# Kernel optimization log

Measured on AMD Instinct MI355X. Metric: run time of the kernel, lower is better.

Reference implementation:

```python
import jax, jax.numpy as jnp
import numpy as np

# dims
B, T1, T2, SEG = 4, 16, 16, 4          # batch, src len, tgt len, max segment length
V, E, H, ENC = 8000, 256, 256, 512     # vocab, embed, lstm hidden, encoder units
EOS = 2                                 # end-of-segment symbol ($)
NEG = -1e30                             # finite -inf (grad-safe)


def setup_inputs():
    key = jax.random.key(0)
    ks = jax.random.split(key, 16)
    s = 0.05
    n = lambda k, shp: (jax.random.normal(k, shp) * s).astype(jnp.float32)
    return {
        "prev_output_tokens": jax.random.randint(ks[0], (B, T2), 0, V),
        "encoder_outs": jax.random.normal(ks[1], (T1, B, ENC), dtype=jnp.float32),
        "embed": n(ks[2], (V, E)),
        "start_embed": n(ks[3], (E,)),
        "proj_h_w": n(ks[4], (H, ENC)), "proj_h_b": jnp.zeros((H,), jnp.float32),
        "proj_c_w": n(ks[5], (H, ENC)), "proj_c_b": jnp.zeros((H,), jnp.float32),
        "w_ih0": n(ks[6], (4 * H, H + E)), "w_hh0": n(ks[7], (4 * H, H)), "b0": jnp.zeros((4 * H,), jnp.float32),
        "w_ih1": n(ks[8], (4 * H, H)), "w_hh1": n(ks[9], (4 * H, H)), "b1": jnp.zeros((4 * H,), jnp.float32),
        "fc_w": n(ks[10], (V, H)), "fc_b": jnp.zeros((V,), jnp.float32),
    }


def _lstm_cell(x, h, c, w_ih, w_hh, b):
    # PyTorch LSTMCell gate order: i, f, g, o
    g = x @ w_ih.T + h @ w_hh.T + b
    i, f, gg, o = jnp.split(g, 4, axis=-1)
    c_new = jax.nn.sigmoid(f) * c + jax.nn.sigmoid(i) * jnp.tanh(gg)
    h_new = jax.nn.sigmoid(o) * jnp.tanh(c_new)
    return h_new, c_new


def reference(prev_output_tokens, encoder_outs, embed, start_embed,
              proj_h_w, proj_h_b, proj_c_w, proj_c_b,
              w_ih0, w_hh0, b0, w_ih1, w_hh1, b1, fc_w, fc_b):
    y = prev_output_tokens                                     # [B, T2]
    # segment windows: tok[b, t2, k] = y[b, t2+k] (clipped; masked later via logpy mask)
    pos = jnp.arange(T2 + 1)[:, None] + jnp.arange(SEG)[None, :]   # [T2+1, SEG]
    tok = y[:, jnp.minimum(pos, T2 - 1)]                            # [B, T2+1, SEG]
    emb_tok = embed[tok]                                            # [B, T2+1, SEG, E]
    x0 = jnp.broadcast_to(start_embed, (B, T2 + 1, 1, E))
    xs = jnp.moveaxis(jnp.concatenate([x0, emb_tok], axis=2), 2, 0)  # [SEG+1, B, T2+1, E]
    tgt = jnp.concatenate([tok, jnp.zeros((B, T2 + 1, 1), tok.dtype)], axis=2)
    tgt = jnp.moveaxis(tgt, 2, 0)                                    # [SEG+1, B, T2+1]

    # per-encoder-position initial states / context (encoder proj, as in __init__)
    eo = jnp.swapaxes(encoder_outs, 0, 1)                            # [B, T1, ENC]
    h0 = eo @ proj_h_w.T + proj_h_b                                  # [B, T1, H]
    c0 = eo @ proj_c_w.T + proj_c_b
    ctx = jnp.broadcast_to(h0[:, :, None, :], (B, T1, T2 + 1, H))

    def step(carry, inp):
        h1, c1, h2, c2 = carry
        x, t = inp                                                   # x [B,T2+1,E], t [B,T2+1]
        xb = jnp.broadcast_to(x[:, None, :, :], (B, T1, T2 + 1, E))
        h1, c1 = _lstm_cell(jnp.concatenate([ctx, xb], axis=-1), h1, c1, w_ih0, w_hh0, b0)
        h2, c2 = _lstm_cell(h1, h2, c2, w_ih1, w_hh1, b1)
        logp = jax.nn.log_softmax(h2 @ fc_w.T + fc_b, axis=-1)       # [B,T1,T2+1,V]
        idx = jnp.broadcast_to(t[:, None, :, None], (B, T1, T2 + 1, 1))
        sel = jnp.take_along_axis(logp, idx, axis=-1)[..., 0]
        return (h1, c1, h2, c2), (sel, logp[..., EOS])

    carry0 = (ctx,
              jnp.broadcast_to(c0[:, :, None, :], (B, T1, T2 + 1, H)),
              jnp.zeros((B, T1, T2 + 1, H), jnp.float32),
              jnp.zeros((B, T1, T2 + 1, H), jnp.float32))
    _, (sel, eosp) = jax.lax.scan(step, carry0, (xs, tgt))           # each [SEG+1,B,T1,T2+1]

    # logpy[b,t1,t2,j] = sum_{k<j} logp_k(y[t2+k]) + logp_j(EOS)
    cum = jnp.concatenate([jnp.zeros((1, B, T1, T2 + 1), sel.dtype),
                           jnp.cumsum(sel[:SEG], axis=0)], axis=0)
    logpy = jnp.moveaxis(cum + eosp, 0, -1)                          # [B,T1,T2+1,SEG+1]
    jmask = (jnp.arange(T2 + 1)[:, None] + jnp.arange(SEG + 1)[None, :]) <= T2
    logpy = jnp.where(jmask[None, None], logpy, NEG)

    # semi-Markov forward DP: alpha[t1+1, t2] = LSE_j alpha[t1, t2-j] + logpy[t1, t2-j, j]
    alpha0 = jnp.full((B, T2 + 1), NEG, sel.dtype).at[:, 0].set(0.0)

    def dp(alpha, row):                                              # row [B, T2+1, SEG+1]
        v = alpha[:, :, None] + row
        shifted = jnp.stack(
            [jnp.pad(v[:, :T2 + 1 - j, j], ((0, 0), (j, 0)), constant_values=NEG)
             for j in range(SEG + 1)], axis=0)
        return jax.nn.logsumexp(shifted, axis=0), None

    alpha, _ = jax.lax.scan(dp, alpha0, jnp.moveaxis(logpy, 1, 0))
    return alpha[:, T2]                                              # log-likelihood per batch elem
```

## Files before the change

kernel.cpp:

```cpp
#include <hip/hip_runtime.h>
#include <math.h>

#define B 4
#define T1 16
#define T2 16
#define SEG 4
#define V 8000
#define E 256
#define H 256
#define ENC 512
#define EOS 2
#define NEGV -1e30f
#define G4 1024
#define NCELL 1088
#define T21 17
#define NL 272
#define MROWS 5440
#define NFCT 10625

typedef __attribute__((ext_vector_type(4))) float f32x4;
typedef __attribute__((ext_vector_type(8))) short bf16x8;

__device__ __forceinline__ float sigm(float x) { return 1.f / (1.f + __expf(-x)); }
__device__ __forceinline__ float ftanh(float x) { float e = __expf(2.f * x); return 1.f - 2.f / (e + 1.f); }
__device__ __forceinline__ float b2f(short x) {
    unsigned u = ((unsigned)(unsigned short)x) << 16;
    return __builtin_bit_cast(float, u);
}
__device__ __forceinline__ short f2b(float f) {
    unsigned u = __builtin_bit_cast(unsigned, f);
    unsigned r = (u + 0x7fffu + ((u >> 16) & 1u)) >> 16;
    return (short)r;
}

__device__ __forceinline__ void stage64(const char* g0, size_t gstrideB, int kOffB, char* lds) {
    int tid = threadIdx.x;
#pragma unroll
    for (int it = 0; it < 8; ++it) {
        int chunk = it * 256 + tid;
        int row = chunk >> 5;
        int c16 = chunk & 31;
        const char* src = g0 + (size_t)row * gstrideB + kOffB + ((c16 ^ (row & 7)) << 4);
        __builtin_amdgcn_global_load_lds((const __attribute__((address_space(1))) void*)src,
                                         (__attribute__((address_space(3))) void*)(lds + chunk * 16),
                                         16, 0, 0);
    }
}

__device__ __forceinline__ bf16x8 lds_frag(const char* lds, int row, int col16) {
    return *(const bf16x8*)(lds + row * 512 + ((col16 ^ (row & 7)) << 4));
}

__device__ __forceinline__ void mma_tile(const char* smA, const char* smB,
                                         int wave, int ln, int kg, f32x4 acc[4]) {
#pragma unroll
    for (int ks = 0; ks < 8; ++ks) {
        bf16x8 a = lds_frag(smA, wave * 16 + ln, ks * 4 + kg);
#pragma unroll
        for (int nf = 0; nf < 4; ++nf) {
            bf16x8 b = lds_frag(smB, nf * 16 + ln, ks * 4 + kg);
            acc[nf] = __builtin_amdgcn_mfma_f32_16x16x32_bf16(a, b, acc[nf], 0, 0, 0);
        }
    }
}

__global__ void k_setup(const float* __restrict__ fcw, const float* __restrict__ whh0,
                        const float* __restrict__ wih1, const float* __restrict__ whh1,
                        const float* __restrict__ phw, const float* __restrict__ pcw,
                        const float* __restrict__ wih0, const float* __restrict__ b1,
                        short* __restrict__ fcwbf, short* __restrict__ whh0i, short* __restrict__ w1i,
                        float* __restrict__ projhT, float* __restrict__ projcT,
                        float* __restrict__ ctxT, float* __restrict__ xT, float* __restrict__ b1i) {
    int bid = blockIdx.x, tid = threadIdx.x;
    if (bid < 8000) { int i = bid * 256 + tid; fcwbf[i] = f2b(fcw[i]); return; }
    bid -= 8000;
    if (bid < 1024) {
        int i = bid * 256 + tid; int gp = i >> 8, k = i & 255; int j = gp >> 2, gate = gp & 3;
        whh0i[i] = f2b(whh0[(size_t)(gate * 256 + j) * 256 + k]); return;
    }
    bid -= 1024;
    if (bid < 2048) {
        int i = bid * 256 + tid; int gp = i >> 9, k = i & 511; int j = gp >> 2, gate = gp & 3;
        float v = (k < 256) ? wih1[(size_t)(gate * 256 + j) * 256 + k]
                            : whh1[(size_t)(gate * 256 + j) * 256 + (k - 256)];
        w1i[i] = f2b(v); return;
    }
    bid -= 2048;
    if (bid < 512) { int i = bid * 256 + tid; int k = i >> 8, r = i & 255; projhT[i] = phw[(size_t)r * ENC + k]; return; }
    bid -= 512;
    if (bid < 512) { int i = bid * 256 + tid; int k = i >> 8, r = i & 255; projcT[i] = pcw[(size_t)r * ENC + k]; return; }
    bid -= 512;
    if (bid < 2048) {
        int i = bid * 256 + tid; int g = i >> 9, k = i & 511; float v = wih0[i];
        if (k < 256) ctxT[(size_t)k * G4 + g] = v; else xT[(size_t)(k - 256) * G4 + g] = v;
        return;
    }
    bid -= 2048;
    if (bid < 4) { int i = bid * 256 + tid; int j = i >> 2, gate = i & 3; b1i[i] = b1[gate * 256 + j]; return; }
}

__global__ void k_init_state(const float* __restrict__ enc, const float* __restrict__ phT,
                             const float* __restrict__ phb, const float* __restrict__ pcT,
                             const float* __restrict__ pcb, float* __restrict__ h0, float* __restrict__ c0) {
    __shared__ float eo[ENC];
    int bi = blockIdx.x;
    int b = bi / T1, i = bi % T1;
    int j = threadIdx.x;
    for (int e = j; e < ENC; e += 256) eo[e] = enc[(size_t)(i * B + b) * ENC + e];
    __syncthreads();
    float ha = phb[j], ca = pcb[j];
    for (int e = 0; e < ENC; ++e) {
        float x = eo[e];
        ha += x * phT[(size_t)e * H + j];
        ca += x * pcT[(size_t)e * H + j];
    }
    h0[(size_t)bi * H + j] = ha;
    c0[(size_t)bi * H + j] = ca;
}

__global__ void k_init2(const int* __restrict__ y, const float* __restrict__ embed, const float* __restrict__ se,
                        const float* __restrict__ h0, const float* __restrict__ c0,
                        const float* __restrict__ ctxT, const float* __restrict__ xT,
                        const float* __restrict__ b0,
                        float* __restrict__ c1, float* __restrict__ c2,
                        short* __restrict__ hcA, short* __restrict__ hcB,
                        float* __restrict__ pre_ctxi, float* __restrict__ pre_xi) {
    __shared__ float sb[256];
    int bid = blockIdx.x, j = threadIdx.x;
    if (bid < NCELL) {
        int cell = bid, bi = cell / T21;
        c1[(size_t)cell * H + j] = c0[(size_t)bi * H + j];
        c2[(size_t)cell * H + j] = 0.f;
        hcA[(size_t)cell * 512 + j] = f2b(h0[(size_t)bi * H + j]);
        hcB[(size_t)cell * 512 + 256 + j] = 0;
        return;
    }
    bid -= NCELL;
    if (bid < 64) {
        int bi = bid;
        sb[j] = h0[(size_t)bi * H + j];
        __syncthreads();
        float a0 = b0[j], a1 = b0[256 + j], a2 = b0[512 + j], a3 = b0[768 + j];
        for (int k = 0; k < H; ++k) {
            float x = sb[k];
            const float* w = ctxT + (size_t)k * G4;
            a0 += x * w[j]; a1 += x * w[256 + j]; a2 += x * w[512 + j]; a3 += x * w[768 + j];
        }
        *(float4*)&pre_ctxi[(size_t)bi * G4 + 4 * j] = make_float4(a0, a1, a2, a3);
        return;
    }
    bid -= 64;
    int row = bid;
    int s = row / (B * T21), rem = row % (B * T21);
    int b = rem / T21, t = rem % T21;
    const float* src;
    if (s == 0) src = se;
    else { int tt = t + s - 1; if (tt > 15) tt = 15; src = embed + (size_t)y[b * T2 + tt] * E; }
    sb[j] = src[j];
    __syncthreads();
    float a0 = 0, a1 = 0, a2 = 0, a3 = 0;
    for (int k = 0; k < E; ++k) {
        float x = sb[k];
        const float* w = xT + (size_t)k * G4;
        a0 += x * w[j]; a1 += x * w[256 + j]; a2 += x * w[512 + j]; a3 += x * w[768 + j];
    }
    *(float4*)&pre_xi[(size_t)row * G4 + 4 * j] = make_float4(a0, a1, a2, a3);
}

__device__ __forceinline__ void lstm0_body(int step, int l, char* smA, char* smB,
        const short* __restrict__ IN, const short* __restrict__ whh0i,
        const float* __restrict__ pre_ctxi, const float* __restrict__ pre_xi,
        float* __restrict__ c1, short* __restrict__ OUT) {
    int tid = threadIdx.x;
    int wave = tid >> 6, lane = tid & 63, ln = lane & 15, kg = lane >> 4;
    int mb = l >> 4, nb = l & 15;
    int m0 = mb * 64, n0 = nb * 64;
    stage64((const char*)(IN + (size_t)m0 * 512), 1024, 0, smA);
    stage64((const char*)(whh0i + (size_t)n0 * 256), 512, 0, smB);
    __syncthreads();
    f32x4 acc[4] = {};
    mma_tile(smA, smB, wave, ln, kg, acc);
    __syncthreads();
    float* sg = (float*)smA;
#pragma unroll
    for (int nf = 0; nf < 4; ++nf)
#pragma unroll
        for (int r = 0; r < 4; ++r)
            sg[(wave * 16 + kg * 4 + r) * 68 + nf * 16 + ln] = acc[nf][r];
    __syncthreads();
    int jlo = nb * 16;
#pragma unroll
    for (int q2 = 0; q2 < 4; ++q2) {
        int item = q2 * 256 + tid;
        int c = item >> 4, jj = item & 15;
        int cell = m0 + c;
        int j = jlo + jj;
        float4 g = *(float4*)&sg[c * 68 + 4 * jj];
        int bi = cell / T21;
        int bb = bi >> 4;
        int t = cell % T21;
        int prow = (step * B + bb) * T21 + t;
        float4 pc = *(const float4*)&pre_ctxi[(size_t)bi * G4 + 4 * j];
        float4 px = *(const float4*)&pre_xi[(size_t)prow * G4 + 4 * j];
        float ig = g.x + pc.x + px.x, fg = g.y + pc.y + px.y;
        float gg = g.z + pc.z + px.z, og = g.w + pc.w + px.w;
        float cold = c1[(size_t)cell * H + j];
        float cn = sigm(fg) * cold + sigm(ig) * ftanh(gg);
        float hn = sigm(og) * ftanh(cn);
        c1[(size_t)cell * H + j] = cn;
        OUT[(size_t)cell * 512 + j] = f2b(hn);
    }
}

__device__ __forceinline__ void lstm1_body(int l, char* smA, char* smB,
        const short* __restrict__ IN, const short* __restrict__ w1i,
        const float* __restrict__ b1i, float* __restrict__ c2,
        short* __restrict__ slab, short* __restrict__ OUT) {
    int tid = threadIdx.x;
    int wave = tid >> 6, lane = tid & 63, ln = lane & 15, kg = lane >> 4;
    int mb = l >> 4, nb = l & 15;
    int m0 = mb * 64, n0 = nb * 64;
    f32x4 acc[4] = {};
#pragma unroll
    for (int kh = 0; kh < 2; ++kh) {
        if (kh) __syncthreads();
        stage64((const char*)(IN + (size_t)m0 * 512), 1024, kh * 512, smA);
        stage64((const char*)(w1i + (size_t)n0 * 512), 1024, kh * 512, smB);
        __syncthreads();
        mma_tile(smA, smB, wave, ln, kg, acc);
    }
    __syncthreads();
    float* sg = (float*)smA;
#pragma unroll
    for (int nf = 0; nf < 4; ++nf)
#pragma unroll
        for (int r = 0; r < 4; ++r)
            sg[(wave * 16 + kg * 4 + r) * 68 + nf * 16 + ln] = acc[nf][r];
    __syncthreads();
    int jlo = nb * 16;
#pragma unroll
    for (int q2 = 0; q2 < 4; ++q2) {
        int item = q2 * 256 + tid;
        int c = item >> 4, jj = item & 15;
        int cell = m0 + c;
        int j = jlo + jj;
        float4 g = *(float4*)&sg[c * 68 + 4 * jj];
        float4 bv = *(const float4*)&b1i[4 * j];
        float ig = g.x + bv.x, fg = g.y + bv.y, gg = g.z + bv.z, og = g.w + bv.w;
        float cold = c2[(size_t)cell * H + j];
        float cn = sigm(fg) * cold + sigm(ig) * ftanh(gg);
        float hn = sigm(og) * ftanh(cn);
        c2[(size_t)cell * H + j] = cn;
        short hb = f2b(hn);
        slab[(size_t)cell * 256 + j] = hb;
        OUT[(size_t)cell * 512 + 256 + j] = hb;
    }
}

__global__ __launch_bounds__(256, 2) void k_lstm(int s, int n_l1,
        const short* __restrict__ IN, short* __restrict__ OUT, short* __restrict__ slab,
        const short* __restrict__ whh0i, const short* __restrict__ w1i,
        const float* __restrict__ pre_ctxi, const float* __restrict__ pre_xi,
        const float* __restrict__ b1i, float* __restrict__ c1, float* __restrict__ c2) {
    __shared__ char smem[65536];
    char* smA = smem;
    char* smB = smem + 32768;
    int bx = blockIdx.x;
    if (bx < n_l1) lstm1_body(bx, smA, smB, IN, w1i, b1i, c2, slab, OUT);
    else lstm0_body(s + 1, bx - n_l1, smA, smB, IN, whh0i, pre_ctxi, pre_xi, c1, OUT);
}

__global__ __launch_bounds__(256, 2) void k_fc(const short* __restrict__ h2base, const short* __restrict__ Wv,
        const float* __restrict__ fcb, float* __restrict__ psum) {
    __shared__ char smem[65536];
    char* smA = smem;
    char* smB = smem + 32768;
    int bx = blockIdx.x;
    int xcd = bx & 7, idx = bx >> 3;
    int q = NFCT >> 3, r = NFCT & 7;
    int l = xcd * q + (xcd < r ? xcd : r) + idx;
    int nb = l / 85, rem = l % 85;
    int s = rem / 17, mb = rem % 17;
    int m0 = s * NCELL + mb * 64;
    int n0 = nb * 64;
    int tid = threadIdx.x;
    int wave = tid >> 6, lane = tid & 63, ln = lane & 15, kg = lane >> 4;
    stage64((const char*)(h2base + (size_t)m0 * 256), 512, 0, smA);
    stage64((const char*)(Wv + (size_t)n0 * 256), 512, 0, smB);
    __syncthreads();
    f32x4 acc[4] = {};
    mma_tile(smA, smB, wave, ln, kg, acc);
    float rs[4] = {0.f, 0.f, 0.f, 0.f};
#pragma unroll
    for (int nf = 0; nf < 4; ++nf) {
        float fbn = fcb[n0 + nf * 16 + ln];
#pragma unroll
        for (int r2 = 0; r2 < 4; ++r2)
            rs[r2] += __expf(acc[nf][r2] + fbn);
    }
#pragma unroll
    for (int mask = 1; mask < 16; mask <<= 1)
#pragma unroll
        for (int r2 = 0; r2 < 4; ++r2)
            rs[r2] += __shfl_xor(rs[r2], mask);
    if (ln == 0) {
#pragma unroll
        for (int r2 = 0; r2 < 4; ++r2)
            psum[(size_t)nb * MROWS + m0 + wave * 16 + kg * 4 + r2] = rs[r2];
    }
}

__global__ void k_combine(const short* __restrict__ h2all, const short* __restrict__ Wv,
        const float* __restrict__ fcb, const int* __restrict__ y,
        const float* __restrict__ psum, float* __restrict__ sel, float* __restrict__ eosp) {
    int cb = blockIdx.x;
    int s = cb / 17, blk = cb % 17;
    int tid = threadIdx.x;
    int cl = tid >> 2, q = tid & 3;
    int cell = blk * 64 + cl;
    int b = cell / (T1 * T21);
    int t = cell % T21;
    int tv = 0;
    if (s < SEG) { int tt = t + s; if (tt > 15) tt = 15; tv = y[b * T2 + tt]; }
    const short* hp = h2all + (size_t)(s + 1) * NCELL * 256 + (size_t)cell * 256 + q * 64;
    const short* w1 = Wv + (size_t)tv * 256 + q * 64;
    const short* w2 = Wv + (size_t)EOS * 256 + q * 64;
    float d1 = 0.f, d2 = 0.f;
#pragma unroll
    for (int u = 0; u < 8; ++u) {
        bf16x8 av  = *(const bf16x8*)(hp + u * 8);
        bf16x8 wv1 = *(const bf16x8*)(w1 + u * 8);
        bf16x8 wv2 = *(const bf16x8*)(w2 + u * 8);
#pragma unroll
        for (int e = 0; e < 8; ++e) {
            float a = b2f(av[e]);
            d1 += a * b2f(wv1[e]);
            d2 += a * b2f(wv2[e]);
        }
    }
    d1 += __shfl_xor(d1, 1); d1 += __shfl_xor(d1, 2);
    d2 += __shfl_xor(d2, 1); d2 += __shfl_xor(d2, 2);
    int col = s * NCELL + cell;
    float ss = 0.f;
    for (int v2 = q * 32; v2 < q * 32 + 32 && v2 < 125; ++v2)
        ss += psum[(size_t)v2 * MROWS + col];
    ss += __shfl_xor(ss, 1); ss += __shfl_xor(ss, 2);
    if (q == 0) {
        float lse = __logf(ss);
        sel[s * NCELL + cell]  = d1 + fcb[tv]  - lse;
        eosp[s * NCELL + cell] = d2 + fcb[EOS] - lse;
    }
}

__global__ void k_dp(const float* __restrict__ sel, const float* __restrict__ eosp, float* __restrict__ out) {
    __shared__ float row[SEG + 1][NCELL];
    __shared__ float alpha[B][T21];
    int tid = threadIdx.x;
    for (int c = tid; c < NCELL; c += 256) {
        float cum = 0.f;
        row[0][c] = eosp[c];
#pragma unroll
        for (int j = 1; j <= SEG; ++j) {
            cum += sel[(j - 1) * NCELL + c];
            row[j][c] = cum + eosp[j * NCELL + c];
        }
    }
    int b = tid / T21, t = tid % T21;
    bool act = tid < B * T21;
    if (act) alpha[b][t] = (t == 0) ? 0.f : NEGV;
    __syncthreads();
    for (int i = 0; i < T1; ++i) {
        float val = NEGV;
        if (act) {
            float terms[SEG + 1];
            float mx = -3.4e38f;
            int cnt2 = 0;
            for (int j = 0; j <= SEG && j <= t; ++j) {
                int cell = (b * T1 + i) * T21 + (t - j);
                float term = alpha[b][t - j] + row[j][cell];
                terms[cnt2++] = term;
                mx = fmaxf(mx, term);
            }
            float ssum = 0.f;
            for (int k2 = 0; k2 < cnt2; ++k2) ssum += __expf(terms[k2] - mx);
            val = mx + __logf(ssum);
        }
        __syncthreads();
        if (act) alpha[b][t] = val;
        __syncthreads();
    }
    if (act && t == T2) out[b] = alpha[b][T2];
}

extern "C" void kernel_launch(void* const* d_in, const int* in_sizes, int n_in,
                              void* d_out, int out_size, void* d_ws, size_t ws_size,
                              hipStream_t stream) {
    const int*   y     = (const int*)d_in[0];
    const float* enc   = (const float*)d_in[1];
    const float* embed = (const float*)d_in[2];
    const float* se    = (const float*)d_in[3];
    const float* phw   = (const float*)d_in[4];
    const float* phb   = (const float*)d_in[5];
    const float* pcw   = (const float*)d_in[6];
    const float* pcb   = (const float*)d_in[7];
    const float* wih0  = (const float*)d_in[8];
    const float* whh0  = (const float*)d_in[9];
    const float* b0    = (const float*)d_in[10];
    const float* wih1  = (const float*)d_in[11];
    const float* whh1  = (const float*)d_in[12];
    const float* b1    = (const float*)d_in[13];
    const float* fcw   = (const float*)d_in[14];
    const float* fcb   = (const float*)d_in[15];

    float* ws = (float*)d_ws;
    size_t off = 0;
    auto alloc = [&](size_t n) { float* p = ws + off; off += n; return p; };
    float* projhT   = alloc((size_t)ENC * H);
    float* projcT   = alloc((size_t)ENC * H);
    float* ctxT     = alloc((size_t)H * G4);
    float* xT       = alloc((size_t)E * G4);
    float* h0       = alloc((size_t)B * T1 * H);
    float* c0       = alloc((size_t)B * T1 * H);
    float* pre_ctxi = alloc((size_t)B * T1 * G4);
    float* pre_xi   = alloc((size_t)(SEG + 1) * B * T21 * G4);
    float* c1       = alloc((size_t)NCELL * H);
    float* c2       = alloc((size_t)NCELL * H);
    float* b1i      = alloc((size_t)G4);
    float* selbuf   = alloc((size_t)(SEG + 1) * NCELL);
    float* eospbuf  = alloc((size_t)(SEG + 1) * NCELL);
    float* psum     = alloc((size_t)125 * MROWS);
    short* hc0      = (short*)alloc((size_t)NCELL * 512 / 2);
    short* hc1      = (short*)alloc((size_t)NCELL * 512 / 2);
    short* h2all    = (short*)alloc((size_t)6 * NCELL * 256 / 2);
    short* whh0i    = (short*)alloc((size_t)G4 * 256 / 2);
    short* w1i      = (short*)alloc((size_t)G4 * 512 / 2);
    short* fcwbf    = (short*)alloc((size_t)V * H / 2);

    hipLaunchKernelGGL(k_setup, dim3(14148), dim3(256), 0, stream,
                       fcw, whh0, wih1, whh1, phw, pcw, wih0, b1,
                       fcwbf, whh0i, w1i, projhT, projcT, ctxT, xT, b1i);
    hipLaunchKernelGGL(k_init_state, dim3(B * T1), dim3(256), 0, stream,
                       enc, projhT, phb, projcT, pcb, h0, c0);
    hipLaunchKernelGGL(k_init2, dim3(NCELL + 64 + (SEG + 1) * B * T21), dim3(256), 0, stream,
                       y, embed, se, h0, c0, ctxT, xT, b0, c1, c2, hc0, hc1,
                       pre_ctxi, pre_xi);

    short* hcb[2] = { hc0, hc1 };
    hipLaunchKernelGGL(k_lstm, dim3(NL), dim3(256), 0, stream,
                       -1, 0, hcb[0], hcb[1], h2all,
                       whh0i, w1i, pre_ctxi, pre_xi, b1i, c1, c2);
    for (int s = 0; s < SEG; ++s) {
        hipLaunchKernelGGL(k_lstm, dim3(2 * NL), dim3(256), 0, stream,
                           s, NL, hcb[(s + 1) & 1], hcb[s & 1],
                           h2all + (size_t)(s + 1) * NCELL * 256,
                           whh0i, w1i, pre_ctxi, pre_xi, b1i, c1, c2);
    }
    hipLaunchKernelGGL(k_lstm, dim3(NL), dim3(256), 0, stream,
                       4, NL, hcb[1], hcb[0],
                       h2all + (size_t)5 * NCELL * 256,
                       whh0i, w1i, pre_ctxi, pre_xi, b1i, c1, c2);

    hipLaunchKernelGGL(k_fc, dim3(NFCT), dim3(256), 0, stream,
                       h2all + (size_t)NCELL * 256, fcwbf, fcb, psum);
    hipLaunchKernelGGL(k_combine, dim3(85), dim3(256), 0, stream,
                       h2all, fcwbf, fcb, y, psum, selbuf, eospbuf);
    hipLaunchKernelGGL(k_dp, dim3(1), dim3(256), 0, stream, selbuf, eospbuf, (float*)d_out);
}
```

Baseline: 201.4 us.

## Retile FC logsumexp GEMM to 128x128 tiles and vectorize setup conversions

The FC partial-softmax GEMM moves from 64x64 tiles with full K staged to 128x128 tiles processed in two K halves. Each wave now computes a 64x64 subtile, which raises operand reuse and cuts the number of tiles and psum partials. Padded vocab columns are masked with a very negative bias, and the LDS swizzle changes to suit 256-byte rows. The setup kernel now converts and transposes weights four elements per thread with float4/short4 accesses, so it launches far fewer blocks. The trade-offs are higher register pressure from 16 accumulators per wave and extra padded rows in h2all.

```diff
diff --git a/kernel.cpp b/kernel.cpp
--- a/kernel.cpp
+++ b/kernel.cpp
@@ -15,8 +15,11 @@
 #define NCELL 1088
 #define T21 17
 #define NL 272
-#define MROWS 5440
-#define NFCT 10625
+#define MP 5504
+#define NTM 43
+#define NTN 63
+#define NFCT (NTM*NTN)
+#define NPART 126
 
 typedef __attribute__((ext_vector_type(4))) float f32x4;
 typedef __attribute__((ext_vector_type(8))) short bf16x8;
@@ -33,24 +36,24 @@
     return (short)r;
 }
 
+__device__ __forceinline__ int swz8(int row) { return (row & 7) ^ ((row & 3) << 1); }
+
 __device__ __forceinline__ void stage64(const char* g0, size_t gstrideB, int kOffB, char* lds) {
     int tid = threadIdx.x;
 #pragma unroll
     for (int it = 0; it < 8; ++it) {
         int chunk = it * 256 + tid;
         int row = chunk >> 5;
-        int c16 = chunk & 31;
-        const char* src = g0 + (size_t)row * gstrideB + kOffB + ((c16 ^ (row & 7)) << 4);
+        int g = chunk & 31;
+        const char* src = g0 + (size_t)row * gstrideB + kOffB + ((g ^ swz8(row)) << 4);
         __builtin_amdgcn_global_load_lds((const __attribute__((address_space(1))) void*)src,
                                          (__attribute__((address_space(3))) void*)(lds + chunk * 16),
                                          16, 0, 0);
     }
 }
-
 __device__ __forceinline__ bf16x8 lds_frag(const char* lds, int row, int col16) {
-    return *(const bf16x8*)(lds + row * 512 + ((col16 ^ (row & 7)) << 4));
-}
-
+    return *(const bf16x8*)(lds + row * 512 + ((col16 ^ swz8(row)) << 4));
+}
 __device__ __forceinline__ void mma_tile(const char* smA, const char* smB,
                                          int wave, int ln, int kg, f32x4 acc[4]) {
 #pragma unroll
@@ -62,6 +65,10 @@
             acc[nf] = __builtin_amdgcn_mfma_f32_16x16x32_bf16(a, b, acc[nf], 0, 0, 0);
         }
     }
+}
+
+__device__ __forceinline__ bf16x8 frag128(const char* lds, int row, int gl) {
+    return *(const bf16x8*)(lds + row * 256 + ((gl ^ swz8(row)) << 4));
 }
 
 __global__ void k_setup(const float* __restrict__ fcw, const float* __restrict__ whh0,
@@ -72,31 +79,66 @@
                         float* __restrict__ projhT, float* __restrict__ projcT,
                         float* __restrict__ ctxT, float* __restrict__ xT, float* __restrict__ b1i) {
     int bid = blockIdx.x, tid = threadIdx.x;
-    if (bid < 8000) { int i = bid * 256 + tid; fcwbf[i] = f2b(fcw[i]); return; }
-    bid -= 8000;
-    if (bid < 1024) {
-        int i = bid * 256 + tid; int gp = i >> 8, k = i & 255; int j = gp >> 2, gate = gp & 3;
-        whh0i[i] = f2b(whh0[(size_t)(gate * 256 + j) * 256 + k]); return;
-    }
-    bid -= 1024;
-    if (bid < 2048) {
-        int i = bid * 256 + tid; int gp = i >> 9, k = i & 511; int j = gp >> 2, gate = gp & 3;
-        float v = (k < 256) ? wih1[(size_t)(gate * 256 + j) * 256 + k]
-                            : whh1[(size_t)(gate * 256 + j) * 256 + (k - 256)];
-        w1i[i] = f2b(v); return;
-    }
-    bid -= 2048;
-    if (bid < 512) { int i = bid * 256 + tid; int k = i >> 8, r = i & 255; projhT[i] = phw[(size_t)r * ENC + k]; return; }
+    if (bid < 2000) {
+        int i = (bid * 256 + tid) * 4;
+        float4 v = *(const float4*)&fcw[i];
+        short4 o = { f2b(v.x), f2b(v.y), f2b(v.z), f2b(v.w) };
+        *(short4*)&fcwbf[i] = o;
+        return;
+    }
+    bid -= 2000;
+    if (bid < 256) {
+        int i = (bid * 256 + tid) * 4;
+        int gp = i >> 8, k = i & 255;
+        float4 v = *(const float4*)&whh0[(size_t)((gp & 3) * 256 + (gp >> 2)) * 256 + k];
+        short4 o = { f2b(v.x), f2b(v.y), f2b(v.z), f2b(v.w) };
+        *(short4*)&whh0i[i] = o;
+        return;
+    }
+    bid -= 256;
+    if (bid < 512) {
+        int i = (bid * 256 + tid) * 4;
+        int gp = i >> 9, k = i & 511;
+        int g = (gp & 3) * 256 + (gp >> 2);
+        const float* src = (k < 256) ? &wih1[(size_t)g * 256 + k] : &whh1[(size_t)g * 256 + (k - 256)];
+        float4 v = *(const float4*)src;
+        short4 o = { f2b(v.x), f2b(v.y), f2b(v.z), f2b(v.w) };
+        *(short4*)&w1i[i] = o;
+        return;
+    }
     bid -= 512;
-    if (bid < 512) { int i = bid * 256 + tid; int k = i >> 8, r = i & 255; projcT[i] = pcw[(size_t)r * ENC + k]; return; }
+    if (bid < 128) {
+        int i = (bid * 256 + tid) * 4;
+        int k = i >> 8, r = i & 255;
+        float4 o = { phw[(size_t)r * ENC + k], phw[(size_t)(r + 1) * ENC + k],
+                     phw[(size_t)(r + 2) * ENC + k], phw[(size_t)(r + 3) * ENC + k] };
+        *(float4*)&projhT[i] = o;
+        return;
+    }
+    bid -= 128;
+    if (bid < 128) {
+        int i = (bid * 256 + tid) * 4;
+        int k = i >> 8, r = i & 255;
+        float4 o = { pcw[(size_t)r * ENC + k], pcw[(size_t)(r + 1) * ENC + k],
+                     pcw[(size_t)(r + 2) * ENC + k], pcw[(size_t)(r + 3) * ENC + k] };
+        *(float4*)&projcT[i] = o;
+        return;
+    }
+    bid -= 128;
+    if (bid < 512) {
+        int i = (bid * 256 + tid) * 4;
+        int g = i >> 9, k = i & 511;
+        float4 v = *(const float4*)&wih0[i];
+        float* base = (k < 256) ? &ctxT[(size_t)k * G4 + g] : &xT[(size_t)(k - 256) * G4 + g];
+        base[0] = v.x; base[G4] = v.y; base[2 * G4] = v.z; base[3 * G4] = v.w;
+        return;
+    }
     bid -= 512;
-    if (bid < 2048) {
-        int i = bid * 256 + tid; int g = i >> 9, k = i & 511; float v = wih0[i];
-        if (k < 256) ctxT[(size_t)k * G4 + g] = v; else xT[(size_t)(k - 256) * G4 + g] = v;
-        return;
-    }
-    bid -= 2048;
-    if (bid < 4) { int i = bid * 256 + tid; int j = i >> 2, gate = i & 3; b1i[i] = b1[gate * 256 + j]; return; }
+    if (bid < 1) {
+        float4 o = { b1[tid], b1[256 + tid], b1[512 + tid], b1[768 + tid] };
+        *(float4*)&b1i[tid * 4] = o;
+        return;
+    }
 }
 
 __global__ void k_init_state(const float* __restrict__ enc, const float* __restrict__ phT,
@@ -278,35 +320,82 @@
     int bx = blockIdx.x;
     int xcd = bx & 7, idx = bx >> 3;
     int q = NFCT >> 3, r = NFCT & 7;
-    int l = xcd * q + (xcd < r ? xcd : r) + idx;
-    int nb = l / 85, rem = l % 85;
-    int s = rem / 17, mb = rem % 17;
-    int m0 = s * NCELL + mb * 64;
-    int n0 = nb * 64;
+    int tl = xcd * q + (xcd < r ? xcd : r) + idx;
+    int nb = tl / NTM, mb = tl % NTM;
+    int m0 = mb * 128, n0 = nb * 128;
     int tid = threadIdx.x;
     int wave = tid >> 6, lane = tid & 63, ln = lane & 15, kg = lane >> 4;
-    stage64((const char*)(h2base + (size_t)m0 * 256), 512, 0, smA);
-    stage64((const char*)(Wv + (size_t)n0 * 256), 512, 0, smB);
-    __syncthreads();
-    f32x4 acc[4] = {};
-    mma_tile(smA, smB, wave, ln, kg, acc);
-    float rs[4] = {0.f, 0.f, 0.f, 0.f};
+    int wm = wave >> 1, wn = wave & 1;
+    f32x4 acc[4][4] = {};
+#pragma unroll
+    for (int kh = 0; kh < 2; ++kh) {
+        if (kh) __syncthreads();
+#pragma unroll
+        for (int it = 0; it < 8; ++it) {
+            int chunk = it * 256 + tid;
+            int row = chunk >> 4;
+            int g = chunk & 15;
+            const char* src = (const char*)(h2base + (size_t)(m0 + row) * 256)
+                              + kh * 256 + ((g ^ swz8(row)) << 4);
+            __builtin_amdgcn_global_load_lds((const __attribute__((address_space(1))) void*)src,
+                                             (__attribute__((address_space(3))) void*)(smA + chunk * 16),
+                                             16, 0, 0);
+        }
+#pragma unroll
+        for (int it = 0; it < 8; ++it) {
+            int chunk = it * 256 + tid;
+            int row = chunk >> 4;
+            int g = chunk & 15;
+            int grow = n0 + row; if (grow > V - 1) grow = V - 1;
+            const char* src = (const char*)(Wv + (size_t)grow * 256)
+                              + kh * 256 + ((g ^ swz8(row)) << 4);
+            __builtin_amdgcn_global_load_lds((const __attribute__((address_space(1))) void*)src,
+                                             (__attribute__((address_space(3))) void*)(smB + chunk * 16),
+                                             16, 0, 0);
+        }
+        __syncthreads();
+#pragma unroll
+        for (int ks = 0; ks < 4; ++ks) {
+            bf16x8 a[4], b[4];
+#pragma unroll
+            for (int mf = 0; mf < 4; ++mf) a[mf] = frag128(smA, wm * 64 + mf * 16 + ln, ks * 4 + kg);
+#pragma unroll
+            for (int nf = 0; nf < 4; ++nf) b[nf] = frag128(smB, wn * 64 + nf * 16 + ln, ks * 4 + kg);
+#pragma unroll
+            for (int mf = 0; mf < 4; ++mf)
+#pragma unroll
+                for (int nf = 0; nf < 4; ++nf)
+                    acc[mf][nf] = __builtin_amdgcn_mfma_f32_16x16x32_bf16(a[mf], b[nf], acc[mf][nf], 0, 0, 0);
+        }
+    }
+    float rs[4][4];
+#pragma unroll
+    for (int mf = 0; mf < 4; ++mf)
+#pragma unroll
+        for (int r2 = 0; r2 < 4; ++r2) rs[mf][r2] = 0.f;
 #pragma unroll
     for (int nf = 0; nf < 4; ++nf) {
-        float fbn = fcb[n0 + nf * 16 + ln];
-#pragma unroll
-        for (int r2 = 0; r2 < 4; ++r2)
-            rs[r2] += __expf(acc[nf][r2] + fbn);
+        int col = n0 + wn * 64 + nf * 16 + ln;
+        float fbn = (col < V) ? fcb[col] : NEGV;
+#pragma unroll
+        for (int mf = 0; mf < 4; ++mf)
+#pragma unroll
+            for (int r2 = 0; r2 < 4; ++r2)
+                rs[mf][r2] += __expf(acc[mf][nf][r2] + fbn);
     }
 #pragma unroll
     for (int mask = 1; mask < 16; mask <<= 1)
 #pragma unroll
-        for (int r2 = 0; r2 < 4; ++r2)
-            rs[r2] += __shfl_xor(rs[r2], mask);
+        for (int mf = 0; mf < 4; ++mf)
+#pragma unroll
+            for (int r2 = 0; r2 < 4; ++r2)
+                rs[mf][r2] += __shfl_xor(rs[mf][r2], mask);
     if (ln == 0) {
 #pragma unroll
-        for (int r2 = 0; r2 < 4; ++r2)
-            psum[(size_t)nb * MROWS + m0 + wave * 16 + kg * 4 + r2] = rs[r2];
+        for (int mf = 0; mf < 4; ++mf)
+#pragma unroll
+            for (int r2 = 0; r2 < 4; ++r2)
+                psum[(size_t)(nb * 2 + wn) * MP + m0 + wm * 64 + mf * 16 + kg * 4 + r2] = rs[mf][r2];
     }
 }
 
@@ -342,8 +431,8 @@
     d2 += __shfl_xor(d2, 1); d2 += __shfl_xor(d2, 2);
     int col = s * NCELL + cell;
     float ss = 0.f;
-    for (int v2 = q * 32; v2 < q * 32 + 32 && v2 < 125; ++v2)
-        ss += psum[(size_t)v2 * MROWS + col];
+    for (int v2 = q * 32; v2 < q * 32 + 32 && v2 < NPART; ++v2)
+        ss += psum[(size_t)v2 * MP + col];
     ss += __shfl_xor(ss, 1); ss += __shfl_xor(ss, 2);
     if (q == 0) {
         float lse = __logf(ss);
@@ -428,15 +517,15 @@
     float* b1i      = alloc((size_t)G4);
     float* selbuf   = alloc((size_t)(SEG + 1) * NCELL);
     float* eospbuf  = alloc((size_t)(SEG + 1) * NCELL);
-    float* psum     = alloc((size_t)125 * MROWS);
+    float* psum     = alloc((size_t)NPART * MP);
     short* hc0      = (short*)alloc((size_t)NCELL * 512 / 2);
     short* hc1      = (short*)alloc((size_t)NCELL * 512 / 2);
-    short* h2all    = (short*)alloc((size_t)6 * NCELL * 256 / 2);
+    short* h2all    = (short*)alloc(((size_t)6 * NCELL + 64) * 256 / 2);
     short* whh0i    = (short*)alloc((size_t)G4 * 256 / 2);
     short* w1i      = (short*)alloc((size_t)G4 * 512 / 2);
     short* fcwbf    = (short*)alloc((size_t)V * H / 2);
 
-    hipLaunchKernelGGL(k_setup, dim3(14148), dim3(256), 0, stream,
+    hipLaunchKernelGGL(k_setup, dim3(3537), dim3(256), 0, stream,
                        fcw, whh0, wih1, whh1, phw, pcw, wih0, b1,
                        fcwbf, whh0i, w1i, projhT, projcT, ctxT, xT, b1i);
     hipLaunchKernelGGL(k_init_state, dim3(B * T1), dim3(256), 0, stream,
```

After: 186.6 us. 1.08x faster.
